# Performance work log

Measured on AMD Instinct MI355X. Metric: run time of the kernel, lower is better.

Reference implementation:

```python
import jax, jax.numpy as jnp
import numpy as np

VOCAB = 30000
FEAT = 30000
HID = 1024
EMB = 1024
B, LQ, LKV = 32, 256, 256


def setup_inputs() -> dict:
    key = jax.random.key(0)
    ks = jax.random.split(key, 8)
    captions = jax.random.randint(ks[0], (B, LKV), 0, VOCAB)
    targets_feature = jax.random.randint(ks[1], (B, LKV), 0, FEAT)
    hidden_state = jax.random.normal(ks[2], (B, LQ, HID), dtype=jnp.float32)
    feature_mask = jax.random.uniform(ks[3], (B, LQ, LKV), dtype=jnp.float32)
    # embeddings initialized uniform(-0.1, 0.1) per init_weights
    Wa = jax.random.uniform(ks[4], (VOCAB, HID), minval=-0.1, maxval=0.1, dtype=jnp.float32)
    Wc = jax.random.uniform(ks[5], (FEAT, HID), minval=-0.1, maxval=0.1, dtype=jnp.float32)
    r = np.sqrt(6.0) / np.sqrt(2 * HID + EMB)
    fc_w = jax.random.uniform(ks[6], (EMB, 2 * HID), minval=-r, maxval=r, dtype=jnp.float32)
    fc_b = jnp.zeros((EMB,), dtype=jnp.float32)
    return {"captions": captions, "hidden_state": hidden_state,
            "targets_feature": targets_feature, "feature_mask": feature_mask,
            "Wa": Wa, "Wc": Wc, "fc_w": fc_w, "fc_b": fc_b}


def reference(captions, hidden_state, targets_feature, feature_mask, Wa, Wc, fc_w, fc_b):
    ea = Wa[captions]           # [B, LKV, H]
    ec = Wc[targets_feature]    # [B, LKV, H]
    # u = hidden_state @ embedding_a^T : [B, LQ, LKV]
    u = jnp.einsum('bqh,bkh->bqk', hidden_state, ea)
    mask = jnp.clip(feature_mask, 0.0, 1.0)
    delta = jnp.exp(u) * mask
    p = delta / (jnp.sum(delta, axis=2, keepdims=True) + 1e-10)  # masked softmax-like weights
    # weighted value sum without materializing [B,LQ,LKV,H] broadcasts
    o = jnp.einsum('bqk,bkh->bqh', p, ec)
    o = jnp.concatenate([hidden_state, o], axis=2)               # [B, LQ, 2H]
    o = o @ fc_w.T + fc_b                                        # [B, LQ, EMB]
    o = o + 1e-10
    norm = jnp.sqrt(jnp.sum(o * o, axis=-1, keepdims=True)) + 1e-8
    return o / norm
```

## Files before the change

kernel.cpp:

```cpp
#include <hip/hip_runtime.h>
#include <hip/hip_bf16.h>

typedef __attribute__((ext_vector_type(8))) short short8;
typedef __attribute__((ext_vector_type(4))) float f32x4;
using bf16 = __hip_bfloat16;


__device__ __forceinline__ void glds16(const void* g, void* lds) {
  __builtin_amdgcn_global_load_lds(
      (const __attribute__((address_space(1))) void*)g,
      (__attribute__((address_space(3))) void*)lds, 16, 0, 0);
}

__global__ __launch_bounds__(256) void k1_convert(
    const int* __restrict__ captions, const float* __restrict__ Wa,
    const float* __restrict__ H, const float* __restrict__ fcw,
    bf16* __restrict__ EA, bf16* __restrict__ X, bf16* __restrict__ FW) {
  int task = blockIdx.x;
  const float* src;
  bf16* dst;
  int n;
  if (task < 8192) {
    src = Wa + (size_t)captions[task] * 1024;
    dst = EA + (size_t)task * 1024;
    n = 1024;
  } else if (task < 16384) {
    int t = task - 8192;
    src = H + (size_t)t * 1024;
    dst = X + (size_t)t * 2048;
    n = 1024;
  } else {
    int t = task - 16384;
    src = fcw + (size_t)t * 2048;
    dst = FW + (size_t)t * 2048;
    n = 2048;
  }
  for (int c = threadIdx.x * 4; c < n; c += 1024) {
    float4 v = *(const float4*)(src + c);
    __hip_bfloat162 p0, p1;
    p0.x = __float2bfloat16(v.x); p0.y = __float2bfloat16(v.y);
    p1.x = __float2bfloat16(v.z); p1.y = __float2bfloat16(v.w);
    *(__hip_bfloat162*)(dst + c) = p0;
    *(__hip_bfloat162*)(dst + c + 2) = p1;
  }
}

__global__ __launch_bounds__(256) void k1b_gather_transpose(
    const int* __restrict__ targets, const float* __restrict__ Wc,
    bf16* __restrict__ ECT) {
  __shared__ float T[64][67];
  int bid = blockIdx.x;
  int b = bid >> 6;
  int kt = (bid >> 4) & 3;
  int ht = bid & 15;
  int tid = threadIdx.x;
#pragma unroll
  for (int p = 0; p < 4; ++p) {
    int k = p * 16 + (tid >> 4);
    int idx = targets[b * 256 + kt * 64 + k];
    const float* s = Wc + (size_t)idx * 1024 + ht * 64 + (tid & 15) * 4;
    float4 v = *(const float4*)s;
    int c = (tid & 15) * 4;
    T[k][c] = v.x; T[k][c + 1] = v.y; T[k][c + 2] = v.z; T[k][c + 3] = v.w;
  }
  __syncthreads();
#pragma unroll
  for (int p = 0; p < 8; ++p) {
    int h = p * 8 + (tid >> 5);
    int k = (tid & 31) * 2;
    __hip_bfloat162 o;
    o.x = __float2bfloat16(T[k][h]);
    o.y = __float2bfloat16(T[k + 1][h]);
    *(__hip_bfloat162*)(ECT + ((size_t)b * 1024 + ht * 64 + h) * 256 + kt * 64 + k) = o;
  }
}

__global__ __launch_bounds__(256) void k2_scores_softmax(
    const bf16* __restrict__ X, const bf16* __restrict__ EA,
    const float* __restrict__ mask, bf16* __restrict__ P) {
  __shared__ __align__(16) bf16 As[64 * 64];
  __shared__ __align__(16) bf16 Bs[256 * 64];
  int b = blockIdx.x >> 2;
  int mb = blockIdx.x & 3;
  int tid = threadIdx.x;
  int w = tid >> 6, l = tid & 63;
  f32x4 acc[16];
  f32x4 zero = {0.f, 0.f, 0.f, 0.f};
#pragma unroll
  for (int n = 0; n < 16; ++n) acc[n] = zero;

  const bf16* Ag = X + ((size_t)b * 256 + mb * 64) * 2048;
  const bf16* Bg = EA + (size_t)b * 256 * 1024;

  for (int kt = 0; kt < 16; ++kt) {
#pragma unroll
    for (int i = 0; i < 2; ++i) {
      int c = i * 256 + tid;
      int row = c >> 3, slot = c & 7;
      int ss = slot ^ (row & 7);
      glds16(Ag + (size_t)row * 2048 + kt * 64 + ss * 8,
             As + (size_t)(i * 256 + w * 64) * 8);
    }
#pragma unroll
    for (int i = 0; i < 8; ++i) {
      int c = i * 256 + tid;
      int row = c >> 3, slot = c & 7;
      int ss = slot ^ (row & 7);
      glds16(Bg + (size_t)row * 1024 + kt * 64 + ss * 8,
             Bs + (size_t)(i * 256 + w * 64) * 8);
    }
    __syncthreads();
#pragma unroll
    for (int kk = 0; kk < 2; ++kk) {
      int arow = w * 16 + (l & 15);
      int aslot = kk * 4 + (l >> 4);
      short8 af = *(const short8*)(As + arow * 64 + ((aslot ^ (arow & 7)) * 8));
#pragma unroll
      for (int n = 0; n < 16; ++n) {
        int brow = n * 16 + (l & 15);
        int bslot = kk * 4 + (l >> 4);
        short8 bfr = *(const short8*)(Bs + brow * 64 + ((bslot ^ (brow & 7)) * 8));
        acc[n] = __builtin_amdgcn_mfma_f32_16x16x32_bf16(af, bfr, acc[n], 0, 0, 0);
      }
    }
    __syncthreads();
  }
  int q0 = mb * 64 + w * 16 + ((l >> 4) << 2);
  const float* mrow = mask + ((size_t)b * 256 + q0) * 256;
  float s[4] = {0.f, 0.f, 0.f, 0.f};
#pragma unroll
  for (int n = 0; n < 16; ++n) {
    int col = (l & 15) + 16 * n;
#pragma unroll
    for (int i = 0; i < 4; ++i) {
      float mv = mrow[i * 256 + col];
      mv = fminf(fmaxf(mv, 0.f), 1.f);
      float ev = expf(acc[n][i]) * mv;
      acc[n][i] = ev;
      s[i] += ev;
    }
  }
#pragma unroll
  for (int m = 1; m < 16; m <<= 1) {
#pragma unroll
    for (int i = 0; i < 4; ++i) s[i] += __shfl_xor(s[i], m, 64);
  }
  bf16* Prow = P + ((size_t)b * 256 + q0) * 256;
#pragma unroll
  for (int i = 0; i < 4; ++i) {
    float inv = 1.f / (s[i] + 1e-10f);
#pragma unroll
    for (int n = 0; n < 16; ++n) {
      int col = (l & 15) + 16 * n;
      Prow[i * 256 + col] = __float2bfloat16(acc[n][i] * inv);
    }
  }
}

__global__ __launch_bounds__(256) void k3_pv(
    const bf16* __restrict__ P, const bf16* __restrict__ ECT,
    bf16* __restrict__ X) {
  __shared__ __align__(16) bf16 As[128 * 64];
  __shared__ __align__(16) bf16 Bs[128 * 64];
  int bid = blockIdx.x;
  int b = bid >> 4;
  int mb = (bid >> 3) & 1;
  int nb = bid & 7;
  int tid = threadIdx.x, w = tid >> 6, l = tid & 63;
  int wr = w >> 1, wc = w & 1;
  f32x4 acc[4][4];
  f32x4 zero = {0.f, 0.f, 0.f, 0.f};
#pragma unroll
  for (int m = 0; m < 4; ++m)
#pragma unroll
    for (int n = 0; n < 4; ++n) acc[m][n] = zero;
  const bf16* Ag = P + (size_t)b * 256 * 256 + mb * 128 * 256;
  const bf16* Bg = ECT + (size_t)b * 1024 * 256 + nb * 128 * 256;
  for (int kt = 0; kt < 4; ++kt) {
#pragma unroll
    for (int i = 0; i < 4; ++i) {
      int c = i * 256 + tid;
      int row = c >> 3, slot = c & 7, ss = slot ^ (row & 7);
      glds16(Ag + (size_t)row * 256 + kt * 64 + ss * 8,
             As + (size_t)(i * 256 + w * 64) * 8);
    }
#pragma unroll
    for (int i = 0; i < 4; ++i) {
      int c = i * 256 + tid;
      int row = c >> 3, slot = c & 7, ss = slot ^ (row & 7);
      glds16(Bg + (size_t)row * 256 + kt * 64 + ss * 8,
             Bs + (size_t)(i * 256 + w * 64) * 8);
    }
    __syncthreads();
#pragma unroll
    for (int kk = 0; kk < 2; ++kk) {
      short8 a[4], bb[4];
#pragma unroll
      for (int m = 0; m < 4; ++m) {
        int row = wr * 64 + m * 16 + (l & 15);
        int slot = kk * 4 + (l >> 4);
        a[m] = *(const short8*)(As + row * 64 + ((slot ^ (row & 7)) * 8));
      }
#pragma unroll
      for (int n = 0; n < 4; ++n) {
        int row = wc * 64 + n * 16 + (l & 15);
        int slot = kk * 4 + (l >> 4);
        bb[n] = *(const short8*)(Bs + row * 64 + ((slot ^ (row & 7)) * 8));
      }
#pragma unroll
      for (int m = 0; m < 4; ++m)
#pragma unroll
        for (int n = 0; n < 4; ++n)
          acc[m][n] = __builtin_amdgcn_mfma_f32_16x16x32_bf16(a[m], bb[n], acc[m][n], 0, 0, 0);
    }
    __syncthreads();
  }
#pragma unroll
  for (int m = 0; m < 4; ++m) {
    int rbase = b * 256 + mb * 128 + wr * 64 + m * 16 + ((l >> 4) << 2);
#pragma unroll
    for (int n = 0; n < 4; ++n) {
      int col = 1024 + nb * 128 + wc * 64 + n * 16 + (l & 15);
#pragma unroll
      for (int i = 0; i < 4; ++i)
        X[(size_t)(rbase + i) * 2048 + col] = __float2bfloat16(acc[m][n][i]);
    }
  }
}

#define K4T (128 * 64)

__device__ __forceinline__ void k4_stage(const bf16* __restrict__ Ag,
                                         const bf16* __restrict__ Bg, int kt,
                                         bf16* As, bf16* Bs, int tid, int w) {
#pragma unroll
  for (int i = 0; i < 4; ++i) {
    int c = i * 256 + tid;
    int row = c >> 3, ss = (c & 7) ^ (row & 7);
    glds16(Ag + (size_t)row * 2048 + kt * 64 + ss * 8,
           As + (size_t)(i * 256 + w * 64) * 8);
  }
#pragma unroll
  for (int i = 0; i < 4; ++i) {
    int c = i * 256 + tid;
    int row = c >> 3, ss = (c & 7) ^ (row & 7);
    glds16(Bg + (size_t)row * 2048 + kt * 64 + ss * 8,
           Bs + (size_t)(i * 256 + w * 64) * 8);
  }
}

__device__ __forceinline__ void k4_tile(const bf16* As, const bf16* Bs,
                                        int wr, int wc, int l,
                                        f32x4 (&acc)[4][4]) {
  short8 a[2][4], b[2][4];
#pragma unroll
  for (int kk = 0; kk < 2; ++kk)
#pragma unroll
    for (int n = 0; n < 4; ++n) {
      int row = wc * 64 + n * 16 + (l & 15);
      int slot = kk * 4 + (l >> 4);
      b[kk][n] = *(const short8*)(Bs + row * 64 + ((slot ^ (row & 7)) * 8));
    }
#pragma unroll
  for (int kk = 0; kk < 2; ++kk)
#pragma unroll
    for (int m = 0; m < 4; ++m) {
      int row = wr * 64 + m * 16 + (l & 15);
      int slot = kk * 4 + (l >> 4);
      a[kk][m] = *(const short8*)(As + row * 64 + ((slot ^ (row & 7)) * 8));
    }
  __builtin_amdgcn_s_setprio(1);
#pragma unroll
  for (int kk = 0; kk < 2; ++kk)
#pragma unroll
    for (int m = 0; m < 4; ++m)
#pragma unroll
      for (int n = 0; n < 4; ++n)
        acc[m][n] = __builtin_amdgcn_mfma_f32_16x16x32_bf16(
            a[kk][m], b[kk][n], acc[m][n], 0, 0, 0);
  __builtin_amdgcn_s_setprio(0);
}

__global__ __launch_bounds__(256, 2) void k4_fc(
    const bf16* __restrict__ X, const bf16* __restrict__ FW,
    const float* __restrict__ fcb, float* __restrict__ out) {
  __shared__ __align__(16) bf16 As[2][K4T];
  __shared__ __align__(16) bf16 Bs[2][K4T];
  int p = blockIdx.x;
  int wg = (p & 7) * 64 + (p >> 3);
  int mb = wg >> 3;
  int nb = wg & 7;
  int tid = threadIdx.x, w = tid >> 6, l = tid & 63;
  int wr = w >> 1, wc = w & 1;
  f32x4 acc[4][4];
  f32x4 zero = {0.f, 0.f, 0.f, 0.f};
#pragma unroll
  for (int m = 0; m < 4; ++m)
#pragma unroll
    for (int n = 0; n < 4; ++n) acc[m][n] = zero;

  const bf16* Ag = X + (size_t)mb * 128 * 2048;
  const bf16* Bg = FW + (size_t)nb * 128 * 2048;

  k4_stage(Ag, Bg, 0, As[0], Bs[0], tid, w);
  __syncthreads();
  for (int t = 0; t < 32; ++t) {
    int cur = t & 1;
    if (t < 31)
      k4_stage(Ag, Bg, t + 1, As[cur ^ 1], Bs[cur ^ 1], tid, w);
    k4_tile(As[cur], Bs[cur], wr, wc, l, acc);
    __syncthreads();
  }

  float bias[4];
#pragma unroll
  for (int n = 0; n < 4; ++n)
    bias[n] = fcb[nb * 128 + wc * 64 + n * 16 + (l & 15)];
#pragma unroll
  for (int m = 0; m < 4; ++m) {
    int rbase = mb * 128 + wr * 64 + m * 16 + ((l >> 4) << 2);
#pragma unroll
    for (int n = 0; n < 4; ++n) {
      int col = nb * 128 + wc * 64 + n * 16 + (l & 15);
#pragma unroll
      for (int i = 0; i < 4; ++i)
        out[(size_t)(rbase + i) * 1024 + col] = acc[m][n][i] + bias[n] + 1e-10f;
    }
  }
}

__global__ __launch_bounds__(256) void k5_norm(float* __restrict__ y) {
  __shared__ float red[4];
  int row = blockIdx.x;
  float* p = y + (size_t)row * 1024;
  int tid = threadIdx.x;
  float4 v = *(const float4*)(p + tid * 4);
  float ss = v.x * v.x + v.y * v.y + v.z * v.z + v.w * v.w;
#pragma unroll
  for (int m = 1; m < 64; m <<= 1) ss += __shfl_xor(ss, m, 64);
  if ((tid & 63) == 0) red[tid >> 6] = ss;
  __syncthreads();
  float tot = red[0] + red[1] + red[2] + red[3];
  float inv = 1.f / (sqrtf(tot) + 1e-8f);
  float4 o;
  o.x = v.x * inv; o.y = v.y * inv; o.z = v.z * inv; o.w = v.w * inv;
  *(float4*)(p + tid * 4) = o;
}

extern "C" void kernel_launch(void* const* d_in, const int* in_sizes, int n_in,
                              void* d_out, int out_size, void* d_ws, size_t ws_size,
                              hipStream_t stream) {
  const int* captions = (const int*)d_in[0];
  const float* H = (const float*)d_in[1];
  const int* targets = (const int*)d_in[2];
  const float* mask = (const float*)d_in[3];
  const float* Wa = (const float*)d_in[4];
  const float* Wc = (const float*)d_in[5];
  const float* fcw = (const float*)d_in[6];
  const float* fcb = (const float*)d_in[7];
  float* out = (float*)d_out;

  char* ws = (char*)d_ws;
  bf16* EA = (bf16*)(ws);
  bf16* ECT = (bf16*)(ws + (16u << 20));
  bf16* P = (bf16*)(ws + (32u << 20));
  bf16* X = (bf16*)(ws + (36u << 20));
  bf16* FW = (bf16*)(ws + (68u << 20));

  k1_convert<<<17408, 256, 0, stream>>>(captions, Wa, H, fcw, EA, X, FW);
  k1b_gather_transpose<<<2048, 256, 0, stream>>>(targets, Wc, ECT);
  k2_scores_softmax<<<128, 256, 0, stream>>>(X, EA, mask, P);
  k3_pv<<<512, 256, 0, stream>>>(P, ECT, X);
  k4_fc<<<512, 256, 0, stream>>>(X, FW, fcb, out);
  k5_norm<<<8192, 256, 0, stream>>>(out);
}
```

Before: 128.1 us.

## Merge prep kernels, add XCD block swizzle, enlarge FC GEMM tile to 256x128

The two prep kernels (gather/convert and gather-transpose) are fused into one launch to remove a kernel launch and its tail. The scores and PV kernels get an XCD-aware block remap so neighbouring work shares an L2. The FC GEMM moves from 128x128 tiles with 256 threads to 256x128 tiles with 512 threads, cutting redundant weight loads. In exchange it halves the block count to 256, so occupancy drops and the tail gets coarser.

```diff
diff --git a/kernel.cpp b/kernel.cpp
--- a/kernel.cpp
+++ b/kernel.cpp
@@ -12,48 +12,48 @@
       (__attribute__((address_space(3))) void*)lds, 16, 0, 0);
 }
 
-__global__ __launch_bounds__(256) void k1_convert(
+__global__ __launch_bounds__(256) void k1_prep(
     const int* __restrict__ captions, const float* __restrict__ Wa,
     const float* __restrict__ H, const float* __restrict__ fcw,
-    bf16* __restrict__ EA, bf16* __restrict__ X, bf16* __restrict__ FW) {
-  int task = blockIdx.x;
-  const float* src;
-  bf16* dst;
-  int n;
-  if (task < 8192) {
-    src = Wa + (size_t)captions[task] * 1024;
-    dst = EA + (size_t)task * 1024;
-    n = 1024;
-  } else if (task < 16384) {
-    int t = task - 8192;
-    src = H + (size_t)t * 1024;
-    dst = X + (size_t)t * 2048;
-    n = 1024;
-  } else {
-    int t = task - 16384;
-    src = fcw + (size_t)t * 2048;
-    dst = FW + (size_t)t * 2048;
-    n = 2048;
-  }
-  for (int c = threadIdx.x * 4; c < n; c += 1024) {
-    float4 v = *(const float4*)(src + c);
-    __hip_bfloat162 p0, p1;
-    p0.x = __float2bfloat16(v.x); p0.y = __float2bfloat16(v.y);
-    p1.x = __float2bfloat16(v.z); p1.y = __float2bfloat16(v.w);
-    *(__hip_bfloat162*)(dst + c) = p0;
-    *(__hip_bfloat162*)(dst + c + 2) = p1;
-  }
-}
-
-__global__ __launch_bounds__(256) void k1b_gather_transpose(
     const int* __restrict__ targets, const float* __restrict__ Wc,
+    bf16* __restrict__ EA, bf16* __restrict__ X, bf16* __restrict__ FW,
     bf16* __restrict__ ECT) {
   __shared__ float T[64][67];
-  int bid = blockIdx.x;
+  int task = blockIdx.x;
+  int tid = threadIdx.x;
+  if (task < 17408) {
+    const float* src;
+    bf16* dst;
+    int n;
+    if (task < 8192) {
+      src = Wa + (size_t)captions[task] * 1024;
+      dst = EA + (size_t)task * 1024;
+      n = 1024;
+    } else if (task < 16384) {
+      int t = task - 8192;
+      src = H + (size_t)t * 1024;
+      dst = X + (size_t)t * 2048;
+      n = 1024;
+    } else {
+      int t = task - 16384;
+      src = fcw + (size_t)t * 2048;
+      dst = FW + (size_t)t * 2048;
+      n = 2048;
+    }
+    for (int c = tid * 4; c < n; c += 1024) {
+      float4 v = *(const float4*)(src + c);
+      __hip_bfloat162 p0, p1;
+      p0.x = __float2bfloat16(v.x); p0.y = __float2bfloat16(v.y);
+      p1.x = __float2bfloat16(v.z); p1.y = __float2bfloat16(v.w);
+      *(__hip_bfloat162*)(dst + c) = p0;
+      *(__hip_bfloat162*)(dst + c + 2) = p1;
+    }
+    return;
+  }
+  int bid = task - 17408;
   int b = bid >> 6;
   int kt = (bid >> 4) & 3;
   int ht = bid & 15;
-  int tid = threadIdx.x;
 #pragma unroll
   for (int p = 0; p < 4; ++p) {
     int k = p * 16 + (tid >> 4);
@@ -80,8 +80,10 @@
     const float* __restrict__ mask, bf16* __restrict__ P) {
   __shared__ __align__(16) bf16 As[64 * 64];
   __shared__ __align__(16) bf16 Bs[256 * 64];
-  int b = blockIdx.x >> 2;
-  int mb = blockIdx.x & 3;
+  int p = blockIdx.x;
+  int wg = (p & 7) * 16 + (p >> 3);
+  int b = wg >> 2;
+  int mb = wg & 3;
   int tid = threadIdx.x;
   int w = tid >> 6, l = tid & 63;
   f32x4 acc[16];
@@ -162,10 +164,11 @@
     bf16* __restrict__ X) {
   __shared__ __align__(16) bf16 As[128 * 64];
   __shared__ __align__(16) bf16 Bs[128 * 64];
-  int bid = blockIdx.x;
-  int b = bid >> 4;
-  int mb = (bid >> 3) & 1;
-  int nb = bid & 7;
+  int p = blockIdx.x;
+  int wg = (p & 7) * 64 + (p >> 3);
+  int b = wg >> 4;
+  int mb = (wg >> 3) & 1;
+  int nb = wg & 7;
   int tid = threadIdx.x, w = tid >> 6, l = tid & 63;
   int wr = w >> 1, wc = w & 1;
   f32x4 acc[4][4];
@@ -228,24 +231,25 @@
   }
 }
 
-#define K4T (128 * 64)
+#define K4A (256 * 64)
+#define K4B (128 * 64)
 
 __device__ __forceinline__ void k4_stage(const bf16* __restrict__ Ag,
                                          const bf16* __restrict__ Bg, int kt,
                                          bf16* As, bf16* Bs, int tid, int w) {
 #pragma unroll
   for (int i = 0; i < 4; ++i) {
-    int c = i * 256 + tid;
+    int c = i * 512 + tid;
     int row = c >> 3, ss = (c & 7) ^ (row & 7);
     glds16(Ag + (size_t)row * 2048 + kt * 64 + ss * 8,
-           As + (size_t)(i * 256 + w * 64) * 8);
-  }
-#pragma unroll
-  for (int i = 0; i < 4; ++i) {
-    int c = i * 256 + tid;
+           As + (size_t)(i * 512 + w * 64) * 8);
+  }
+#pragma unroll
+  for (int i = 0; i < 2; ++i) {
+    int c = i * 512 + tid;
     int row = c >> 3, ss = (c & 7) ^ (row & 7);
     glds16(Bg + (size_t)row * 2048 + kt * 64 + ss * 8,
-           Bs + (size_t)(i * 256 + w * 64) * 8);
+           Bs + (size_t)(i * 512 + w * 64) * 8);
   }
 }
 
@@ -281,13 +285,13 @@
   __builtin_amdgcn_s_setprio(0);
 }
 
-__global__ __launch_bounds__(256, 2) void k4_fc(
+__global__ __launch_bounds__(512, 1) void k4_fc(
     const bf16* __restrict__ X, const bf16* __restrict__ FW,
     const float* __restrict__ fcb, float* __restrict__ out) {
-  __shared__ __align__(16) bf16 As[2][K4T];
-  __shared__ __align__(16) bf16 Bs[2][K4T];
+  __shared__ __align__(16) bf16 As[2][K4A];
+  __shared__ __align__(16) bf16 Bs[2][K4B];
   int p = blockIdx.x;
-  int wg = (p & 7) * 64 + (p >> 3);
+  int wg = (p & 7) * 32 + (p >> 3);
   int mb = wg >> 3;
   int nb = wg & 7;
   int tid = threadIdx.x, w = tid >> 6, l = tid & 63;
@@ -299,7 +303,7 @@
 #pragma unroll
     for (int n = 0; n < 4; ++n) acc[m][n] = zero;
 
-  const bf16* Ag = X + (size_t)mb * 128 * 2048;
+  const bf16* Ag = X + (size_t)mb * 256 * 2048;
   const bf16* Bg = FW + (size_t)nb * 128 * 2048;
 
   k4_stage(Ag, Bg, 0, As[0], Bs[0], tid, w);
@@ -318,7 +322,7 @@
     bias[n] = fcb[nb * 128 + wc * 64 + n * 16 + (l & 15)];
 #pragma unroll
   for (int m = 0; m < 4; ++m) {
-    int rbase = mb * 128 + wr * 64 + m * 16 + ((l >> 4) << 2);
+    int rbase = mb * 256 + wr * 64 + m * 16 + ((l >> 4) << 2);
 #pragma unroll
     for (int n = 0; n < 4; ++n) {
       int col = nb * 128 + wc * 64 + n * 16 + (l & 15);
@@ -367,10 +371,10 @@
   bf16* X = (bf16*)(ws + (36u << 20));
   bf16* FW = (bf16*)(ws + (68u << 20));
 
-  k1_convert<<<17408, 256, 0, stream>>>(captions, Wa, H, fcw, EA, X, FW);
-  k1b_gather_transpose<<<2048, 256, 0, stream>>>(targets, Wc, ECT);
+  k1_prep<<<19456, 256, 0, stream>>>(captions, Wa, H, fcw, targets, Wc,
+                                     EA, X, FW, ECT);
   k2_scores_softmax<<<128, 256, 0, stream>>>(X, EA, mask, P);
   k3_pv<<<512, 256, 0, stream>>>(P, ECT, X);
-  k4_fc<<<512, 256, 0, stream>>>(X, FW, fcb, out);
+  k4_fc<<<256, 512, 0, stream>>>(X, FW, fcb, out);
   k5_norm<<<8192, 256, 0, stream>>>(out);
 }
```

Result: no change. 128.7 us (+0.4%).
